# Kernel optimization log

Hardware: AMD Instinct MI355X
Metric: run time of the kernel (lower is better)

Reference implementation:

```python
import jax, jax.numpy as jnp
import numpy as np

WINDOW = 5
MAX_LEVELS = 4
EPS = 1e-6

_SX = (jnp.array([[-1., 0., 1.], [-2., 0., 2.], [-1., 0., 1.]], dtype=jnp.float32) / 8.0).reshape(1, 1, 3, 3)
_SY = jnp.transpose(_SX, (0, 1, 3, 2))
_DN = ('NCHW', 'OIHW', 'NCHW')


def _avg_pool2(x):
    B, C, H, W = x.shape
    return x.reshape(B, C, H // 2, 2, W // 2, 2).mean(axis=(3, 5))


def _warp(img, flow):
    # bilinear grid_sample, align_corners=True, zeros padding; sample at pixel coords grid+flow
    B, C, H, W = img.shape
    ys, xs = jnp.meshgrid(jnp.arange(H, dtype=img.dtype), jnp.arange(W, dtype=img.dtype), indexing='ij')
    x = xs[None] + flow[:, 0]  # [B,H,W]
    y = ys[None] + flow[:, 1]
    x0f, y0f = jnp.floor(x), jnp.floor(y)
    wx, wy = x - x0f, y - y0f
    imf = img.reshape(B, C, H * W)

    def gather(yi, xi):
        valid = (xi >= 0) & (xi <= W - 1) & (yi >= 0) & (yi <= H - 1)
        xi_c = jnp.clip(xi, 0, W - 1).astype(jnp.int32)
        yi_c = jnp.clip(yi, 0, H - 1).astype(jnp.int32)
        flat = (yi_c * W + xi_c).reshape(B, 1, H * W)
        v = jnp.take_along_axis(imf, jnp.broadcast_to(flat, (B, C, H * W)), axis=2).reshape(B, C, H, W)
        return v * valid[:, None].astype(img.dtype)

    out = (gather(y0f, x0f) * ((1 - wx) * (1 - wy))[:, None]
           + gather(y0f, x0f + 1) * (wx * (1 - wy))[:, None]
           + gather(y0f + 1, x0f) * ((1 - wx) * wy)[:, None]
           + gather(y0f + 1, x0f + 1) * (wx * wy)[:, None])
    return out


def _resize_ac(x, Hn, Wn):
    # bilinear resize, align_corners=True (static shapes)
    B, C, H, W = x.shape
    if (H, W) == (Hn, Wn):
        return x
    ys = jnp.linspace(0.0, H - 1, Hn, dtype=x.dtype)
    xs = jnp.linspace(0.0, W - 1, Wn, dtype=x.dtype)
    y0 = jnp.clip(jnp.floor(ys), 0, H - 2).astype(jnp.int32)
    x0 = jnp.clip(jnp.floor(xs), 0, W - 2).astype(jnp.int32)
    wy = (ys - y0)[None, None, :, None]
    wx = (xs - x0)[None, None, None, :]
    rows = x[:, :, y0, :] * (1 - wy) + x[:, :, y0 + 1, :] * wy
    return rows[:, :, :, x0] * (1 - wx) + rows[:, :, :, x0 + 1] * wx


def _lucas_kanade(I1, I2):
    if I1.shape[1] > 1:
        I1 = I1.mean(1, keepdims=True)
        I2 = I2.mean(1, keepdims=True)
    Ix = jax.lax.conv_general_dilated(I1, _SX, (1, 1), [(1, 1), (1, 1)], dimension_numbers=_DN)
    Iy = jax.lax.conv_general_dilated(I1, _SY, (1, 1), [(1, 1), (1, 1)], dimension_numbers=_DN)
    It = I2 - I1
    # stack all 5 structure-tensor products and box-filter them with one grouped conv
    stats = jnp.concatenate([Ix * Ix, Iy * Iy, Ix * Iy, Ix * It, Iy * It], axis=1)  # [B,5,H,W]
    boxk = jnp.ones((5, 1, WINDOW, WINDOW), dtype=I1.dtype)
    p0 = WINDOW // 2
    p1 = WINDOW - p0 - 1
    S = jax.lax.conv_general_dilated(stats, boxk, (1, 1), [(p0, p1), (p0, p1)],
                                     feature_group_count=5, dimension_numbers=_DN)
    Sxx, Syy, Sxy, Sxt, Syt = jnp.split(S, 5, axis=1)
    inv = 1.0 / (Sxx * Syy - Sxy * Sxy + EPS)
    u = (-Syy * Sxt + Sxy * Syt) * inv
    v = (Sxy * Sxt - Sxx * Syt) * inv
    return jnp.concatenate([u, v], axis=1)


def setup_inputs() -> dict:
    key = jax.random.key(0)
    k1, k2 = jax.random.split(key)
    img1 = jax.random.uniform(k1, (8, 3, 512, 512), dtype=jnp.float32)
    img2 = jax.random.uniform(k2, (8, 3, 512, 512), dtype=jnp.float32)
    return {"img1": img1, "img2": img2}


def reference(img1, img2):
    B, C, H, W = img1.shape
    levels = max(1, MAX_LEVELS)
    pyr1, pyr2 = [img1], [img2]
    for _ in range(1, levels):
        pyr1.append(_avg_pool2(pyr1[-1]))
        pyr2.append(_avg_pool2(pyr2[-1]))
    flow = jnp.zeros((B, 2, pyr1[-1].shape[2], pyr1[-1].shape[3]), dtype=img1.dtype)
    for lvl in range(levels - 1, -1, -1):
        I1, I2 = pyr1[lvl], pyr2[lvl]
        if lvl < levels - 1:
            flow = _resize_ac(flow, I1.shape[2], I1.shape[3]) * 2.0
        I2w = _warp(I2, flow)
        flow = flow + _lucas_kanade(I1, I2w)
    if flow.shape[2:] != (H, W):
        fh, fw = flow.shape[2], flow.shape[3]
        flow = _resize_ac(flow, H, W)
        flow = flow * jnp.array([W / fw, H / fh], dtype=flow.dtype).reshape(1, 2, 1, 1)
    return flow
```

## Files before the change

kernel.cpp:

```cpp
#include <hip/hip_runtime.h>

#define NB 8
#define TS 16
#define PR 20
#define GR 22
#define SW 24

typedef float f2 __attribute__((ext_vector_type(2)));

__global__ void gray_pool_kernel(const float* __restrict__ img1, const float* __restrict__ img2,
                                 float* __restrict__ g0a, float* __restrict__ g0b,
                                 float* __restrict__ g1a, float* __restrict__ g1b) {
    const int W = 512, HW = 512 * 512, Wq = 256, HWq = 256 * 256;
    int i = blockIdx.x * blockDim.x + threadIdx.x;
    if (i >= NB * HWq) return;
    int qx = i % Wq;
    int qy = (i / Wq) % Wq;
    int b = i / HWq;
    size_t base = (size_t)b * 3 * HW + (size_t)(2 * qy) * W + 2 * qx;
    const float third = 1.0f / 3.0f;

    f2 a0c0 = __builtin_nontemporal_load((const f2*)(img1 + base));
    f2 a1c0 = __builtin_nontemporal_load((const f2*)(img1 + base + W));
    f2 a0c1 = __builtin_nontemporal_load((const f2*)(img1 + base + HW));
    f2 a1c1 = __builtin_nontemporal_load((const f2*)(img1 + base + HW + W));
    f2 a0c2 = __builtin_nontemporal_load((const f2*)(img1 + base + 2 * HW));
    f2 a1c2 = __builtin_nontemporal_load((const f2*)(img1 + base + 2 * HW + W));
    float p00 = (a0c0.x + a0c1.x + a0c2.x) * third;
    float p01 = (a0c0.y + a0c1.y + a0c2.y) * third;
    float p10 = (a1c0.x + a1c1.x + a1c2.x) * third;
    float p11 = (a1c0.y + a1c1.y + a1c2.y) * third;
    size_t gbase = (size_t)b * HW + (size_t)(2 * qy) * W + 2 * qx;
    *(f2*)(g0a + gbase) = (f2){p00, p01};
    *(f2*)(g0a + gbase + W) = (f2){p10, p11};
    g1a[(size_t)b * HWq + qy * Wq + qx] = (p00 + p01 + p10 + p11) * 0.25f;

    f2 b0c0 = __builtin_nontemporal_load((const f2*)(img2 + base));
    f2 b1c0 = __builtin_nontemporal_load((const f2*)(img2 + base + W));
    f2 b0c1 = __builtin_nontemporal_load((const f2*)(img2 + base + HW));
    f2 b1c1 = __builtin_nontemporal_load((const f2*)(img2 + base + HW + W));
    f2 b0c2 = __builtin_nontemporal_load((const f2*)(img2 + base + 2 * HW));
    f2 b1c2 = __builtin_nontemporal_load((const f2*)(img2 + base + 2 * HW + W));
    float q00 = (b0c0.x + b0c1.x + b0c2.x) * third;
    float q01 = (b0c0.y + b0c1.y + b0c2.y) * third;
    float q10 = (b1c0.x + b1c1.x + b1c2.x) * third;
    float q11 = (b1c0.y + b1c1.y + b1c2.y) * third;
    *(f2*)(g0b + gbase) = (f2){q00, q01};
    *(f2*)(g0b + gbase + W) = (f2){q10, q11};
    g1b[(size_t)b * HWq + qy * Wq + qx] = (q00 + q01 + q10 + q11) * 0.25f;
}

__global__ void down2_kernel(const float* __restrict__ l1a, const float* __restrict__ l1b,
                             float* __restrict__ l2a, float* __restrict__ l2b,
                             float* __restrict__ l3a, float* __restrict__ l3b) {
    const int W3 = 64, W2 = 128, W1 = 256;
    int i = blockIdx.x * blockDim.x + threadIdx.x;
    int total = 2 * NB * W3 * W3;
    if (i >= total) return;
    int x3 = i % W3;
    int y3 = (i / W3) % W3;
    int b = (i / (W3 * W3)) % NB;
    int j = i / (NB * W3 * W3);
    const float* l1 = (j ? l1b : l1a) + (size_t)b * W1 * W1;
    float* l2 = (j ? l2b : l2a) + (size_t)b * W2 * W2;
    float* l3 = (j ? l3b : l3a) + (size_t)b * W3 * W3;
    float4 r0 = *(const float4*)(l1 + (size_t)(4 * y3 + 0) * W1 + 4 * x3);
    float4 r1 = *(const float4*)(l1 + (size_t)(4 * y3 + 1) * W1 + 4 * x3);
    float4 r2 = *(const float4*)(l1 + (size_t)(4 * y3 + 2) * W1 + 4 * x3);
    float4 r3 = *(const float4*)(l1 + (size_t)(4 * y3 + 3) * W1 + 4 * x3);
    float a00 = (r0.x + r0.y + r1.x + r1.y) * 0.25f;
    float a01 = (r0.z + r0.w + r1.z + r1.w) * 0.25f;
    float a10 = (r2.x + r2.y + r3.x + r3.y) * 0.25f;
    float a11 = (r2.z + r2.w + r3.z + r3.w) * 0.25f;
    *(f2*)(l2 + (size_t)(2 * y3) * W2 + 2 * x3) = (f2){a00, a01};
    *(f2*)(l2 + (size_t)(2 * y3 + 1) * W2 + 2 * x3) = (f2){a10, a11};
    l3[y3 * W3 + x3] = (a00 + a01 + a10 + a11) * 0.25f;
}

template <int MODE>
__global__ __launch_bounds__(256) void lk_kernel(
    const float* __restrict__ g1, const float* __restrict__ g2,
    const float* __restrict__ fin, float* __restrict__ fout, int H, int W) {
    __shared__ float sG[GR][SW];
    __shared__ float sU[PR][SW], sV[PR][SW];
    __shared__ float sP[5][PR][SW];
    __shared__ float sH[5][PR][16];

    int nbx = W / TS;
    int b = blockIdx.x % NB;
    int t = blockIdx.x / NB;
    int ty0 = (t / nbx) * TS, tx0 = (t % nbx) * TS;
    int tid = threadIdx.x;
    int lx = tid % TS, ly = tid / TS;

    const float* G1 = g1 + (size_t)b * H * W;
    const float* G2 = g2 + (size_t)b * H * W;
    bool interior = (ty0 >= 3) && (ty0 + TS + 3 <= H) && (tx0 >= 3) && (tx0 + TS + 3 <= W);

    if (interior) {
        for (int i = tid; i < GR * GR; i += 256) {
            int r = i / GR, c = i % GR;
            sG[r][c] = G1[(ty0 - 3 + r) * W + (tx0 - 3 + c)];
        }
    } else {
        for (int i = tid; i < GR * GR; i += 256) {
            int r = i / GR, c = i % GR;
            int gy = ty0 - 3 + r, gx = tx0 - 3 + c;
            float v = 0.0f;
            if (gy >= 0 && gy < H && gx >= 0 && gx < W) v = G1[gy * W + gx];
            sG[r][c] = v;
        }
    }
    if (MODE == 1) {
        int Hs = H >> 1, Ws = W >> 1;
        float scale = (float)(Hs - 1) / (float)(H - 1);
        const float* FU = fin + (size_t)b * 2 * Hs * Ws;
        const float* FV = FU + Hs * Ws;
        for (int i = tid; i < PR * PR; i += 256) {
            int r = i / PR, c = i % PR;
            int gy = ty0 - 2 + r, gx = tx0 - 2 + c;
            float sy = (float)gy * scale;
            float sx = (float)gx * scale;
            int y0 = min(max((int)sy, 0), Hs - 2);
            int x0 = min(max((int)sx, 0), Ws - 2);
            float wy = sy - (float)y0, wx = sx - (float)x0;
            const float* pu = FU + (size_t)y0 * Ws + x0;
            const float* pv = FV + (size_t)y0 * Ws + x0;
            float ut = pu[0] * (1.0f - wy) + pu[Ws] * wy;
            float ub = pu[1] * (1.0f - wy) + pu[Ws + 1] * wy;
            float vt = pv[0] * (1.0f - wy) + pv[Ws] * wy;
            float vb = pv[1] * (1.0f - wy) + pv[Ws + 1] * wy;
            sU[r][c] = 2.0f * (ut * (1.0f - wx) + ub * wx);
            sV[r][c] = 2.0f * (vt * (1.0f - wx) + vb * wx);
        }
    } else {
        for (int i = tid; i < PR * PR; i += 256) {
            int r = i / PR, c = i % PR;
            sU[r][c] = 0.0f;
            sV[r][c] = 0.0f;
        }
    }
    __syncthreads();

#pragma unroll
    for (int it = 0; it < 2; ++it) {
        int i = tid + it * 256;
        if (i < PR * PR) {
            int r = i / PR, c = i % PR;
            int gy = ty0 - 2 + r, gx = tx0 - 2 + c;
            float su = sU[r][c], sv = sV[r][c];
            float xx = (float)gx + su, yy = (float)gy + sv;
            float x0f = floorf(xx), y0f = floorf(yy);
            float wx = xx - x0f, wy = yy - y0f;
            int xi = (int)x0f, yi = (int)y0f;
            int xc0 = min(max(xi, 0), W - 1), xc1 = min(max(xi + 1, 0), W - 1);
            int yc0 = min(max(yi, 0), H - 1), yc1 = min(max(yi + 1, 0), H - 1);
            float v00 = G2[yc0 * W + xc0];
            float v01 = G2[yc0 * W + xc1];
            float v10 = G2[yc1 * W + xc0];
            float v11 = G2[yc1 * W + xc1];
            float Wm1 = (float)(W - 1), Hm1 = (float)(H - 1);
            float mx0 = (x0f >= 0.0f && x0f <= Wm1) ? 1.0f : 0.0f;
            float mx1 = (x0f + 1.0f >= 0.0f && x0f + 1.0f <= Wm1) ? 1.0f : 0.0f;
            float my0 = (y0f >= 0.0f && y0f <= Hm1) ? 1.0f : 0.0f;
            float my1 = (y0f + 1.0f >= 0.0f && y0f + 1.0f <= Hm1) ? 1.0f : 0.0f;
            float Ix = (-sG[r][c] + sG[r][c + 2]
                        - 2.0f * sG[r + 1][c] + 2.0f * sG[r + 1][c + 2]
                        - sG[r + 2][c] + sG[r + 2][c + 2]) * 0.125f;
            float Iy = (-sG[r][c] - 2.0f * sG[r][c + 1] - sG[r][c + 2]
                        + sG[r + 2][c] + 2.0f * sG[r + 2][c + 1] + sG[r + 2][c + 2]) * 0.125f;
            float I2w = v00 * ((1.0f - wx) * (1.0f - wy) * mx0 * my0)
                      + v01 * (wx * (1.0f - wy) * mx1 * my0)
                      + v10 * ((1.0f - wx) * wy * mx0 * my1)
                      + v11 * (wx * wy * mx1 * my1);
            float It = I2w - sG[r + 1][c + 1];
            float vm = (interior || (gy >= 0 && gy < H && gx >= 0 && gx < W)) ? 1.0f : 0.0f;
            Ix *= vm; Iy *= vm; It *= vm;
            sP[0][r][c] = Ix * Ix;
            sP[1][r][c] = Iy * Iy;
            sP[2][r][c] = Ix * Iy;
            sP[3][r][c] = Ix * It;
            sP[4][r][c] = Iy * It;
        }
    }
    __syncthreads();

    for (int i = tid; i < 5 * PR * 16; i += 256) {
        int x = i % 16;
        int tt = i / 16;
        int r = tt % PR;
        int ch = tt / PR;
        const float* row = &sP[ch][r][x];
        sH[ch][r][x] = row[0] + row[1] + row[2] + row[3] + row[4];
    }
    __syncthreads();

    float Sxx = 0.f, Syy = 0.f, Sxy = 0.f, Sxt = 0.f, Syt = 0.f;
#pragma unroll
    for (int dy = 0; dy < 5; ++dy) {
        Sxx += sH[0][ly + dy][lx];
        Syy += sH[1][ly + dy][lx];
        Sxy += sH[2][ly + dy][lx];
        Sxt += sH[3][ly + dy][lx];
        Syt += sH[4][ly + dy][lx];
    }
    float inv = 1.0f / (Sxx * Syy - Sxy * Sxy + 1e-6f);
    float du = (-Syy * Sxt + Sxy * Syt) * inv;
    float dv = (Sxy * Sxt - Sxx * Syt) * inv;
    int gy = ty0 + ly, gx = tx0 + lx;
    float* FOU = fout + (size_t)b * 2 * H * W;
    FOU[gy * W + gx] = sU[ly + 2][lx + 2] + du;
    FOU[H * W + gy * W + gx] = sV[ly + 2][lx + 2] + dv;
}

extern "C" void kernel_launch(void* const* d_in, const int* in_sizes, int n_in,
                              void* d_out, int out_size, void* d_ws, size_t ws_size,
                              hipStream_t stream) {
    const float* img1 = (const float*)d_in[0];
    const float* img2 = (const float*)d_in[1];
    float* out = (float*)d_out;
    float* ws = (float*)d_ws;

    const int Hl[4] = {512, 256, 128, 64};
    size_t goff[4];
    size_t tot = 0;
    for (int l = 0; l < 4; ++l) {
        goff[l] = tot;
        tot += (size_t)NB * Hl[l] * Hl[l];
    }
    float* p1 = ws;
    float* p2 = ws + tot;
    float* f64 = p2 + tot;
    float* f128 = f64 + (size_t)NB * 2 * 64 * 64;
    float* f256 = f128 + (size_t)NB * 2 * 128 * 128;

    {
        int n = NB * 256 * 256;
        gray_pool_kernel<<<(n + 255) / 256, 256, 0, stream>>>(
            img1, img2, p1 + goff[0], p2 + goff[0], p1 + goff[1], p2 + goff[1]);
    }
    {
        int n = 2 * NB * 64 * 64;
        down2_kernel<<<(n + 255) / 256, 256, 0, stream>>>(
            p1 + goff[1], p2 + goff[1], p1 + goff[2], p2 + goff[2], p1 + goff[3], p2 + goff[3]);
    }
    {
        int nb = NB * (64 / TS) * (64 / TS);
        lk_kernel<0><<<nb, 256, 0, stream>>>(p1 + goff[3], p2 + goff[3], nullptr, f64, 64, 64);
    }
    {
        int nb = NB * (128 / TS) * (128 / TS);
        lk_kernel<1><<<nb, 256, 0, stream>>>(p1 + goff[2], p2 + goff[2], f64, f128, 128, 128);
    }
    {
        int nb = NB * (256 / TS) * (256 / TS);
        lk_kernel<1><<<nb, 256, 0, stream>>>(p1 + goff[1], p2 + goff[1], f128, f256, 256, 256);
    }
    {
        int nb = NB * (512 / TS) * (512 / TS);
        lk_kernel<1><<<nb, 256, 0, stream>>>(p1 + goff[0], p2 + goff[0], f256, out, 512, 512);
    }
}
```

Baseline: 70.85 us.

## Stage coarse flow patch in LDS, fuse upsampling into warp pass, specialize sizes

The coarse flow patch needed by each tile is now loaded once into shared memory, and the bilinear upsampling is computed inside the warp loop instead of in a separate pass over global memory. This drops one barrier-separated phase and repeated global gathers. Image sizes become template parameters so index math folds to constants. A fast path skips clamping and masking when the bilinear footprint is fully in bounds. The cost is extra shared memory and branch divergence at the borders.

```diff
diff --git a/kernel.cpp b/kernel.cpp
--- a/kernel.cpp
+++ b/kernel.cpp
@@ -5,6 +5,7 @@
 #define PR 20
 #define GR 22
 #define SW 24
+#define SFW 12
 
 typedef float f2 __attribute__((ext_vector_type(2)));
 
@@ -77,16 +78,20 @@
     l3[y3 * W3 + x3] = (a00 + a01 + a10 + a11) * 0.25f;
 }
 
-template <int MODE>
+template <int MODE, int H, int W>
 __global__ __launch_bounds__(256) void lk_kernel(
     const float* __restrict__ g1, const float* __restrict__ g2,
-    const float* __restrict__ fin, float* __restrict__ fout, int H, int W) {
+    const float* __restrict__ fin, float* __restrict__ fout) {
     __shared__ float sG[GR][SW];
     __shared__ float sU[PR][SW], sV[PR][SW];
     __shared__ float sP[5][PR][SW];
     __shared__ float sH[5][PR][16];
-
-    int nbx = W / TS;
+    __shared__ float sFU[SFW][SFW + 1], sFV[SFW][SFW + 1];
+
+    constexpr int nbx = W / TS;
+    constexpr int Hs = H / 2, Ws = W / 2;
+    constexpr float scale = (float)(Hs - 1) / (float)(H - 1);
+
     int b = blockIdx.x % NB;
     int t = blockIdx.x / NB;
     int ty0 = (t / nbx) * TS, tx0 = (t % nbx) * TS;
@@ -97,6 +102,21 @@
     const float* G2 = g2 + (size_t)b * H * W;
     bool interior = (ty0 >= 3) && (ty0 + TS + 3 <= H) && (tx0 >= 3) && (tx0 + TS + 3 <= W);
 
+    int yA = 0, xA = 0;
+    if (MODE == 1) {
+        yA = min(max((int)((float)max(ty0 - 2, 0) * scale), 0), Hs - 2);
+        xA = min(max((int)((float)max(tx0 - 2, 0) * scale), 0), Ws - 2);
+        const float* FU = fin + (size_t)b * 2 * Hs * Ws;
+        const float* FV = FU + Hs * Ws;
+        for (int i = tid; i < 2 * SFW * SFW; i += 256) {
+            int ch = i / (SFW * SFW);
+            int rem = i % (SFW * SFW);
+            int r = rem / SFW, c = rem % SFW;
+            int ys = min(yA + r, Hs - 1), xs = min(xA + c, Ws - 1);
+            float v = (ch ? FV : FU)[(size_t)ys * Ws + xs];
+            if (ch) sFV[r][c] = v; else sFU[r][c] = v;
+        }
+    }
     if (interior) {
         for (int i = tid; i < GR * GR; i += 256) {
             int r = i / GR, c = i % GR;
@@ -111,35 +131,6 @@
             sG[r][c] = v;
         }
     }
-    if (MODE == 1) {
-        int Hs = H >> 1, Ws = W >> 1;
-        float scale = (float)(Hs - 1) / (float)(H - 1);
-        const float* FU = fin + (size_t)b * 2 * Hs * Ws;
-        const float* FV = FU + Hs * Ws;
-        for (int i = tid; i < PR * PR; i += 256) {
-            int r = i / PR, c = i % PR;
-            int gy = ty0 - 2 + r, gx = tx0 - 2 + c;
-            float sy = (float)gy * scale;
-            float sx = (float)gx * scale;
-            int y0 = min(max((int)sy, 0), Hs - 2);
-            int x0 = min(max((int)sx, 0), Ws - 2);
-            float wy = sy - (float)y0, wx = sx - (float)x0;
-            const float* pu = FU + (size_t)y0 * Ws + x0;
-            const float* pv = FV + (size_t)y0 * Ws + x0;
-            float ut = pu[0] * (1.0f - wy) + pu[Ws] * wy;
-            float ub = pu[1] * (1.0f - wy) + pu[Ws + 1] * wy;
-            float vt = pv[0] * (1.0f - wy) + pv[Ws] * wy;
-            float vb = pv[1] * (1.0f - wy) + pv[Ws + 1] * wy;
-            sU[r][c] = 2.0f * (ut * (1.0f - wx) + ub * wx);
-            sV[r][c] = 2.0f * (vt * (1.0f - wx) + vb * wx);
-        }
-    } else {
-        for (int i = tid; i < PR * PR; i += 256) {
-            int r = i / PR, c = i % PR;
-            sU[r][c] = 0.0f;
-            sV[r][c] = 0.0f;
-        }
-    }
     __syncthreads();
 
 #pragma unroll
@@ -148,34 +139,60 @@
         if (i < PR * PR) {
             int r = i / PR, c = i % PR;
             int gy = ty0 - 2 + r, gx = tx0 - 2 + c;
-            float su = sU[r][c], sv = sV[r][c];
+            float su = 0.0f, sv = 0.0f;
+            if (MODE == 1) {
+                float sy = (float)gy * scale, sx = (float)gx * scale;
+                int y0 = min(max((int)sy, 0), Hs - 2);
+                int x0 = min(max((int)sx, 0), Ws - 2);
+                float wyf = sy - (float)y0, wxf = sx - (float)x0;
+                int ry = y0 - yA, rx = x0 - xA;
+                float ut = sFU[ry][rx] * (1.0f - wyf) + sFU[ry + 1][rx] * wyf;
+                float ub = sFU[ry][rx + 1] * (1.0f - wyf) + sFU[ry + 1][rx + 1] * wyf;
+                float vt = sFV[ry][rx] * (1.0f - wyf) + sFV[ry + 1][rx] * wyf;
+                float vb = sFV[ry][rx + 1] * (1.0f - wyf) + sFV[ry + 1][rx + 1] * wyf;
+                su = 2.0f * (ut * (1.0f - wxf) + ub * wxf);
+                sv = 2.0f * (vt * (1.0f - wxf) + vb * wxf);
+            }
+            sU[r][c] = su;
+            sV[r][c] = sv;
+
             float xx = (float)gx + su, yy = (float)gy + sv;
             float x0f = floorf(xx), y0f = floorf(yy);
             float wx = xx - x0f, wy = yy - y0f;
             int xi = (int)x0f, yi = (int)y0f;
-            int xc0 = min(max(xi, 0), W - 1), xc1 = min(max(xi + 1, 0), W - 1);
-            int yc0 = min(max(yi, 0), H - 1), yc1 = min(max(yi + 1, 0), H - 1);
-            float v00 = G2[yc0 * W + xc0];
-            float v01 = G2[yc0 * W + xc1];
-            float v10 = G2[yc1 * W + xc0];
-            float v11 = G2[yc1 * W + xc1];
-            float Wm1 = (float)(W - 1), Hm1 = (float)(H - 1);
-            float mx0 = (x0f >= 0.0f && x0f <= Wm1) ? 1.0f : 0.0f;
-            float mx1 = (x0f + 1.0f >= 0.0f && x0f + 1.0f <= Wm1) ? 1.0f : 0.0f;
-            float my0 = (y0f >= 0.0f && y0f <= Hm1) ? 1.0f : 0.0f;
-            float my1 = (y0f + 1.0f >= 0.0f && y0f + 1.0f <= Hm1) ? 1.0f : 0.0f;
+            float I2w;
+            bool safe = (xi >= 0) && (xi <= W - 2) && (yi >= 0) && (yi <= H - 2);
+            if (__builtin_expect(safe, 1)) {
+                const float* p = G2 + yi * W + xi;
+                float v00 = p[0], v01 = p[1], v10 = p[W], v11 = p[W + 1];
+                float omwx = 1.0f - wx, omwy = 1.0f - wy;
+                I2w = (v00 * omwx + v01 * wx) * omwy + (v10 * omwx + v11 * wx) * wy;
+            } else {
+                int xc0 = min(max(xi, 0), W - 1), xc1 = min(max(xi + 1, 0), W - 1);
+                int yc0 = min(max(yi, 0), H - 1), yc1 = min(max(yi + 1, 0), H - 1);
+                float v00 = G2[yc0 * W + xc0];
+                float v01 = G2[yc0 * W + xc1];
+                float v10 = G2[yc1 * W + xc0];
+                float v11 = G2[yc1 * W + xc1];
+                float mx0 = (x0f >= 0.0f && x0f <= (float)(W - 1)) ? 1.0f : 0.0f;
+                float mx1 = (x0f + 1.0f >= 0.0f && x0f + 1.0f <= (float)(W - 1)) ? 1.0f : 0.0f;
+                float my0 = (y0f >= 0.0f && y0f <= (float)(H - 1)) ? 1.0f : 0.0f;
+                float my1 = (y0f + 1.0f >= 0.0f && y0f + 1.0f <= (float)(H - 1)) ? 1.0f : 0.0f;
+                I2w = v00 * ((1.0f - wx) * (1.0f - wy) * mx0 * my0)
+                    + v01 * (wx * (1.0f - wy) * mx1 * my0)
+                    + v10 * ((1.0f - wx) * wy * mx0 * my1)
+                    + v11 * (wx * wy * mx1 * my1);
+            }
             float Ix = (-sG[r][c] + sG[r][c + 2]
                         - 2.0f * sG[r + 1][c] + 2.0f * sG[r + 1][c + 2]
                         - sG[r + 2][c] + sG[r + 2][c + 2]) * 0.125f;
             float Iy = (-sG[r][c] - 2.0f * sG[r][c + 1] - sG[r][c + 2]
                         + sG[r + 2][c] + 2.0f * sG[r + 2][c + 1] + sG[r + 2][c + 2]) * 0.125f;
-            float I2w = v00 * ((1.0f - wx) * (1.0f - wy) * mx0 * my0)
-                      + v01 * (wx * (1.0f - wy) * mx1 * my0)
-                      + v10 * ((1.0f - wx) * wy * mx0 * my1)
-                      + v11 * (wx * wy * mx1 * my1);
             float It = I2w - sG[r + 1][c + 1];
-            float vm = (interior || (gy >= 0 && gy < H && gx >= 0 && gx < W)) ? 1.0f : 0.0f;
-            Ix *= vm; Iy *= vm; It *= vm;
+            if (!interior) {
+                float vm = (gy >= 0 && gy < H && gx >= 0 && gx < W) ? 1.0f : 0.0f;
+                Ix *= vm; Iy *= vm; It *= vm;
+            }
             sP[0][r][c] = Ix * Ix;
             sP[1][r][c] = Iy * Iy;
             sP[2][r][c] = Ix * Iy;
@@ -246,18 +263,18 @@
     }
     {
         int nb = NB * (64 / TS) * (64 / TS);
-        lk_kernel<0><<<nb, 256, 0, stream>>>(p1 + goff[3], p2 + goff[3], nullptr, f64, 64, 64);
+        lk_kernel<0, 64, 64><<<nb, 256, 0, stream>>>(p1 + goff[3], p2 + goff[3], nullptr, f64);
     }
     {
         int nb = NB * (128 / TS) * (128 / TS);
-        lk_kernel<1><<<nb, 256, 0, stream>>>(p1 + goff[2], p2 + goff[2], f64, f128, 128, 128);
+        lk_kernel<1, 128, 128><<<nb, 256, 0, stream>>>(p1 + goff[2], p2 + goff[2], f64, f128);
     }
     {
         int nb = NB * (256 / TS) * (256 / TS);
-        lk_kernel<1><<<nb, 256, 0, stream>>>(p1 + goff[1], p2 + goff[1], f128, f256, 256, 256);
+        lk_kernel<1, 256, 256><<<nb, 256, 0, stream>>>(p1 + goff[1], p2 + goff[1], f128, f256);
     }
     {
         int nb = NB * (512 / TS) * (512 / TS);
-        lk_kernel<1><<<nb, 256, 0, stream>>>(p1 + goff[0], p2 + goff[0], f256, out, 512, 512);
-    }
-}
+        lk_kernel<1, 512, 512><<<nb, 256, 0, stream>>>(p1 + goff[0], p2 + goff[0], f256, out);
+    }
+}
```

New measurement: 70.53 us. Within noise of the previous version (-0.5%).

## Replace shared-memory LK tiles with per-wavefront rolling-row register kernel

Applied to the files above, without the earlier changes.

The Lucas-Kanade level kernel changes from 16x16 shared-memory tiles with halo recomputation to wavefront-wide 58-column strips. Each strip rolls down TH rows, keeps the vertical window in registers and does the horizontal sums with lane shuffles. This removes the shared-memory staging, the block barriers and most of the halo overhead. It also templates H and W so they are compile-time constants. The costs are full unrolling of the row loop, register pressure, about 10% redundant lanes per strip, and a serial per-row dependency chain within each wave.

```diff
diff --git a/kernel.cpp b/kernel.cpp
--- a/kernel.cpp
+++ b/kernel.cpp
@@ -1,10 +1,6 @@
 #include <hip/hip_runtime.h>
 
 #define NB 8
-#define TS 16
-#define PR 20
-#define GR 22
-#define SW 24
 
 typedef float f2 __attribute__((ext_vector_type(2)));
 
@@ -77,140 +73,151 @@
     l3[y3 * W3 + x3] = (a00 + a01 + a10 + a11) * 0.25f;
 }
 
-template <int MODE>
-__global__ __launch_bounds__(256) void lk_kernel(
+template <int MODE, int H, int W, int TH>
+__global__ __launch_bounds__(256, 4) void lk_roll(
     const float* __restrict__ g1, const float* __restrict__ g2,
-    const float* __restrict__ fin, float* __restrict__ fout, int H, int W) {
-    __shared__ float sG[GR][SW];
-    __shared__ float sU[PR][SW], sV[PR][SW];
-    __shared__ float sP[5][PR][SW];
-    __shared__ float sH[5][PR][16];
-
-    int nbx = W / TS;
-    int b = blockIdx.x % NB;
-    int t = blockIdx.x / NB;
-    int ty0 = (t / nbx) * TS, tx0 = (t % nbx) * TS;
-    int tid = threadIdx.x;
-    int lx = tid % TS, ly = tid / TS;
+    const float* __restrict__ fin, float* __restrict__ fout) {
+    constexpr int XT = (W + 57) / 58;
+    constexpr int YT = H / TH;
+    constexpr int TILES = XT * YT;
+    constexpr int Hs = H / 2, Ws = W / 2;
+    constexpr float scale = (float)(Hs - 1) / (float)(H - 1);
+
+    const int lane = threadIdx.x & 63;
+    const int wid = threadIdx.x >> 6;
+    const int b = blockIdx.x % NB;
+    const int tix = (blockIdx.x / NB) * 4 + wid;
+    if (tix >= TILES) return;
+    const int xt = tix % XT, yt = tix / XT;
+    const int x = xt * 58 - 3 + lane;
+    const bool xin = (x >= 0) && (x < W);
 
     const float* G1 = g1 + (size_t)b * H * W;
     const float* G2 = g2 + (size_t)b * H * W;
-    bool interior = (ty0 >= 3) && (ty0 + TS + 3 <= H) && (tx0 >= 3) && (tx0 + TS + 3 <= W);
-
-    if (interior) {
-        for (int i = tid; i < GR * GR; i += 256) {
-            int r = i / GR, c = i % GR;
-            sG[r][c] = G1[(ty0 - 3 + r) * W + (tx0 - 3 + c)];
+    float* FO = fout + (size_t)b * 2 * H * W;
+
+    int cx0 = 0;
+    float wxf = 0.0f;
+    const float* FU = nullptr;
+    const float* FV = nullptr;
+    if (MODE) {
+        FU = fin + (size_t)b * 2 * Hs * Ws;
+        FV = FU + Hs * Ws;
+        float sx = (float)x * scale;
+        cx0 = min(max((int)sx, 0), Ws - 2);
+        wxf = sx - (float)cx0;
+    }
+
+    const int p0 = yt * TH - 2;
+
+    auto loadrow = [&](int yy, float& g, float& d, float& s) {
+        float gv = (xin && yy >= 0 && yy < H) ? G1[yy * W + x] : 0.0f;
+        float gl = __shfl_up(gv, 1);
+        float gr = __shfl_down(gv, 1);
+        g = gv;
+        d = gr - gl;
+        s = gl + 2.0f * gv + gr;
+    };
+    auto hs5 = [&](float v) {
+        float a = __shfl_down(v, 1);
+        float c = __shfl_down(v, 2);
+        float t = v + a + c;
+        return __shfl_up(t, 2) + a + c;
+    };
+
+    float hxx[5], hyy[5], hxy[5], hxt[5], hyt[5];
+#pragma unroll
+    for (int k = 0; k < 5; ++k) { hxx[k] = hyy[k] = hxy[k] = hxt[k] = hyt[k] = 0.0f; }
+    float su1 = 0.f, su2 = 0.f, sv1 = 0.f, sv2 = 0.f;
+
+    float gm, g0, dm, d0, sm, s0, gp, dp, sp;
+    loadrow(p0 - 1, gm, dm, sm);
+    loadrow(p0, g0, d0, s0);
+
+#pragma unroll
+    for (int i = 0; i < TH + 4; ++i) {
+        const int yc = p0 + i;
+        loadrow(yc + 1, gp, dp, sp);
+        float Ix = (dm + 2.0f * d0 + dp) * 0.125f;
+        float Iy = (sp - sm) * 0.125f;
+
+        float su = 0.0f, sv = 0.0f;
+        if (MODE) {
+            float sy = (float)yc * scale;
+            int y0i = min(max((int)sy, 0), Hs - 2);
+            float wyf = sy - (float)y0i;
+            const float* pu = FU + y0i * Ws + cx0;
+            const float* pv = FV + y0i * Ws + cx0;
+            float u00 = pu[0], u01 = pu[1], u10 = pu[Ws], u11 = pu[Ws + 1];
+            float v00 = pv[0], v01 = pv[1], v10 = pv[Ws], v11 = pv[Ws + 1];
+            float ut = u00 + (u10 - u00) * wyf;
+            float ub = u01 + (u11 - u01) * wyf;
+            float vt = v00 + (v10 - v00) * wyf;
+            float vb = v01 + (v11 - v01) * wyf;
+            su = 2.0f * (ut + (ub - ut) * wxf);
+            sv = 2.0f * (vt + (vb - vt) * wxf);
         }
-    } else {
-        for (int i = tid; i < GR * GR; i += 256) {
-            int r = i / GR, c = i % GR;
-            int gy = ty0 - 3 + r, gx = tx0 - 3 + c;
-            float v = 0.0f;
-            if (gy >= 0 && gy < H && gx >= 0 && gx < W) v = G1[gy * W + gx];
-            sG[r][c] = v;
+
+        float I2w;
+        if (MODE) {
+            float xx = (float)x + su, yy2 = (float)yc + sv;
+            float x0f = floorf(xx), y0f = floorf(yy2);
+            float wx = xx - x0f, wy = yy2 - y0f;
+            int xi = (int)x0f, yi = (int)y0f;
+            int xa = min(max(xi, 0), W - 1), xb = min(max(xi + 1, 0), W - 1);
+            int ya = min(max(yi, 0), H - 1), yb = min(max(yi + 1, 0), H - 1);
+            float w00 = G2[ya * W + xa];
+            float w01 = G2[ya * W + xb];
+            float w10 = G2[yb * W + xa];
+            float w11 = G2[yb * W + xb];
+            float mx0 = (xi >= 0 && xi < W) ? 1.0f : 0.0f;
+            float mx1 = (xi >= -1 && xi < W - 1) ? 1.0f : 0.0f;
+            float my0 = (yi >= 0 && yi < H) ? 1.0f : 0.0f;
+            float my1 = (yi >= -1 && yi < H - 1) ? 1.0f : 0.0f;
+            I2w = w00 * ((1.0f - wx) * (1.0f - wy) * mx0 * my0)
+                + w01 * (wx * (1.0f - wy) * mx1 * my0)
+                + w10 * ((1.0f - wx) * wy * mx0 * my1)
+                + w11 * (wx * wy * mx1 * my1);
+        } else {
+            I2w = (xin && yc >= 0 && yc < H) ? G2[yc * W + x] : 0.0f;
         }
-    }
-    if (MODE == 1) {
-        int Hs = H >> 1, Ws = W >> 1;
-        float scale = (float)(Hs - 1) / (float)(H - 1);
-        const float* FU = fin + (size_t)b * 2 * Hs * Ws;
-        const float* FV = FU + Hs * Ws;
-        for (int i = tid; i < PR * PR; i += 256) {
-            int r = i / PR, c = i % PR;
-            int gy = ty0 - 2 + r, gx = tx0 - 2 + c;
-            float sy = (float)gy * scale;
-            float sx = (float)gx * scale;
-            int y0 = min(max((int)sy, 0), Hs - 2);
-            int x0 = min(max((int)sx, 0), Ws - 2);
-            float wy = sy - (float)y0, wx = sx - (float)x0;
-            const float* pu = FU + (size_t)y0 * Ws + x0;
-            const float* pv = FV + (size_t)y0 * Ws + x0;
-            float ut = pu[0] * (1.0f - wy) + pu[Ws] * wy;
-            float ub = pu[1] * (1.0f - wy) + pu[Ws + 1] * wy;
-            float vt = pv[0] * (1.0f - wy) + pv[Ws] * wy;
-            float vb = pv[1] * (1.0f - wy) + pv[Ws + 1] * wy;
-            sU[r][c] = 2.0f * (ut * (1.0f - wx) + ub * wx);
-            sV[r][c] = 2.0f * (vt * (1.0f - wx) + vb * wx);
+        float It = I2w - g0;
+        float vm = (xin && yc >= 0 && yc < H) ? 1.0f : 0.0f;
+        Ix *= vm; Iy *= vm; It *= vm;
+
+        const int k = i % 5;
+        hxx[k] = Ix * Ix;
+        hyy[k] = Iy * Iy;
+        hxy[k] = Ix * Iy;
+        hxt[k] = Ix * It;
+        hyt[k] = Iy * It;
+
+        if (i >= 4) {
+            float vxx = hxx[0] + hxx[1] + hxx[2] + hxx[3] + hxx[4];
+            float vyy = hyy[0] + hyy[1] + hyy[2] + hyy[3] + hyy[4];
+            float vxy = hxy[0] + hxy[1] + hxy[2] + hxy[3] + hxy[4];
+            float vxt = hxt[0] + hxt[1] + hxt[2] + hxt[3] + hxt[4];
+            float vyt = hyt[0] + hyt[1] + hyt[2] + hyt[3] + hyt[4];
+            float Sxx = hs5(vxx);
+            float Syy = hs5(vyy);
+            float Sxy = hs5(vxy);
+            float Sxt = hs5(vxt);
+            float Syt = hs5(vyt);
+            float inv = 1.0f / (Sxx * Syy - Sxy * Sxy + 1e-6f);
+            float du = (-Syy * Sxt + Sxy * Syt) * inv;
+            float dv = (Sxy * Sxt - Sxx * Syt) * inv;
+            int yo = yc - 2;
+            if (lane >= 3 && lane <= 60 && x < W) {
+                FO[yo * W + x] = su2 + du;
+                FO[H * W + yo * W + x] = sv2 + dv;
+            }
         }
-    } else {
-        for (int i = tid; i < PR * PR; i += 256) {
-            int r = i / PR, c = i % PR;
-            sU[r][c] = 0.0f;
-            sV[r][c] = 0.0f;
-        }
-    }
-    __syncthreads();
-
-#pragma unroll
-    for (int it = 0; it < 2; ++it) {
-        int i = tid + it * 256;
-        if (i < PR * PR) {
-            int r = i / PR, c = i % PR;
-            int gy = ty0 - 2 + r, gx = tx0 - 2 + c;
-            float su = sU[r][c], sv = sV[r][c];
-            float xx = (float)gx + su, yy = (float)gy + sv;
-            float x0f = floorf(xx), y0f = floorf(yy);
-            float wx = xx - x0f, wy = yy - y0f;
-            int xi = (int)x0f, yi = (int)y0f;
-            int xc0 = min(max(xi, 0), W - 1), xc1 = min(max(xi + 1, 0), W - 1);
-            int yc0 = min(max(yi, 0), H - 1), yc1 = min(max(yi + 1, 0), H - 1);
-            float v00 = G2[yc0 * W + xc0];
-            float v01 = G2[yc0 * W + xc1];
-            float v10 = G2[yc1 * W + xc0];
-            float v11 = G2[yc1 * W + xc1];
-            float Wm1 = (float)(W - 1), Hm1 = (float)(H - 1);
-            float mx0 = (x0f >= 0.0f && x0f <= Wm1) ? 1.0f : 0.0f;
-            float mx1 = (x0f + 1.0f >= 0.0f && x0f + 1.0f <= Wm1) ? 1.0f : 0.0f;
-            float my0 = (y0f >= 0.0f && y0f <= Hm1) ? 1.0f : 0.0f;
-            float my1 = (y0f + 1.0f >= 0.0f && y0f + 1.0f <= Hm1) ? 1.0f : 0.0f;
-            float Ix = (-sG[r][c] + sG[r][c + 2]
-                        - 2.0f * sG[r + 1][c] + 2.0f * sG[r + 1][c + 2]
-                        - sG[r + 2][c] + sG[r + 2][c + 2]) * 0.125f;
-            float Iy = (-sG[r][c] - 2.0f * sG[r][c + 1] - sG[r][c + 2]
-                        + sG[r + 2][c] + 2.0f * sG[r + 2][c + 1] + sG[r + 2][c + 2]) * 0.125f;
-            float I2w = v00 * ((1.0f - wx) * (1.0f - wy) * mx0 * my0)
-                      + v01 * (wx * (1.0f - wy) * mx1 * my0)
-                      + v10 * ((1.0f - wx) * wy * mx0 * my1)
-                      + v11 * (wx * wy * mx1 * my1);
-            float It = I2w - sG[r + 1][c + 1];
-            float vm = (interior || (gy >= 0 && gy < H && gx >= 0 && gx < W)) ? 1.0f : 0.0f;
-            Ix *= vm; Iy *= vm; It *= vm;
-            sP[0][r][c] = Ix * Ix;
-            sP[1][r][c] = Iy * Iy;
-            sP[2][r][c] = Ix * Iy;
-            sP[3][r][c] = Ix * It;
-            sP[4][r][c] = Iy * It;
-        }
-    }
-    __syncthreads();
-
-    for (int i = tid; i < 5 * PR * 16; i += 256) {
-        int x = i % 16;
-        int tt = i / 16;
-        int r = tt % PR;
-        int ch = tt / PR;
-        const float* row = &sP[ch][r][x];
-        sH[ch][r][x] = row[0] + row[1] + row[2] + row[3] + row[4];
-    }
-    __syncthreads();
-
-    float Sxx = 0.f, Syy = 0.f, Sxy = 0.f, Sxt = 0.f, Syt = 0.f;
-#pragma unroll
-    for (int dy = 0; dy < 5; ++dy) {
-        Sxx += sH[0][ly + dy][lx];
-        Syy += sH[1][ly + dy][lx];
-        Sxy += sH[2][ly + dy][lx];
-        Sxt += sH[3][ly + dy][lx];
-        Syt += sH[4][ly + dy][lx];
-    }
-    float inv = 1.0f / (Sxx * Syy - Sxy * Sxy + 1e-6f);
-    float du = (-Syy * Sxt + Sxy * Syt) * inv;
-    float dv = (Sxy * Sxt - Sxx * Syt) * inv;
-    int gy = ty0 + ly, gx = tx0 + lx;
-    float* FOU = fout + (size_t)b * 2 * H * W;
-    FOU[gy * W + gx] = sU[ly + 2][lx + 2] + du;
-    FOU[H * W + gy * W + gx] = sV[ly + 2][lx + 2] + dv;
+        su2 = su1; su1 = su;
+        sv2 = sv1; sv1 = sv;
+        gm = g0; g0 = gp;
+        dm = d0; d0 = dp;
+        sm = s0; s0 = sp;
+    }
 }
 
 extern "C" void kernel_launch(void* const* d_in, const int* in_sizes, int n_in,
@@ -245,19 +252,23 @@
             p1 + goff[1], p2 + goff[1], p1 + goff[2], p2 + goff[2], p1 + goff[3], p2 + goff[3]);
     }
     {
-        int nb = NB * (64 / TS) * (64 / TS);
-        lk_kernel<0><<<nb, 256, 0, stream>>>(p1 + goff[3], p2 + goff[3], nullptr, f64, 64, 64);
-    }
-    {
-        int nb = NB * (128 / TS) * (128 / TS);
-        lk_kernel<1><<<nb, 256, 0, stream>>>(p1 + goff[2], p2 + goff[2], f64, f128, 128, 128);
-    }
-    {
-        int nb = NB * (256 / TS) * (256 / TS);
-        lk_kernel<1><<<nb, 256, 0, stream>>>(p1 + goff[1], p2 + goff[1], f128, f256, 256, 256);
-    }
-    {
-        int nb = NB * (512 / TS) * (512 / TS);
-        lk_kernel<1><<<nb, 256, 0, stream>>>(p1 + goff[0], p2 + goff[0], f256, out, 512, 512);
-    }
-}
+        const int tiles = 2 * 8;
+        lk_roll<0, 64, 64, 8><<<NB * ((tiles + 3) / 4), 256, 0, stream>>>(
+            p1 + goff[3], p2 + goff[3], nullptr, f64);
+    }
+    {
+        const int tiles = 3 * 16;
+        lk_roll<1, 128, 128, 8><<<NB * ((tiles + 3) / 4), 256, 0, stream>>>(
+            p1 + goff[2], p2 + goff[2], f64, f128);
+    }
+    {
+        const int tiles = 5 * 32;
+        lk_roll<1, 256, 256, 8><<<NB * ((tiles + 3) / 4), 256, 0, stream>>>(
+            p1 + goff[1], p2 + goff[1], f128, f256);
+    }
+    {
+        const int tiles = 9 * 64;
+        lk_roll<1, 512, 512, 8><<<NB * ((tiles + 3) / 4), 256, 0, stream>>>(
+            p1 + goff[0], p2 + goff[0], f256, out);
+    }
+}
```

Result: slower. 80.68 us (+13.9%).
